# Performance work log

Measured on AMD Instinct MI355X. Metric: run time of the kernel, lower is better.

The kernel has to match this reference:

```python
import jax, jax.numpy as jnp
import numpy as np

EMBED_DIM = 1024
NUM_HEADS = 16
HEAD_DIM = EMBED_DIM // NUM_HEADS
B, T = 4, 1024
NEG = -1.0e9
LN_EPS = 1e-5


def setup_inputs() -> dict:
    key = jax.random.key(0)
    ks = jax.random.split(key, 13)
    s = 1.0 / np.sqrt(EMBED_DIM)
    return {
        "query": jax.random.normal(ks[0], (B, T, EMBED_DIM), jnp.float32),
        "key": jax.random.normal(ks[1], (B, T, EMBED_DIM), jnp.float32),
        "value": jax.random.normal(ks[2], (B, T, EMBED_DIM), jnp.float32),
        "mask": jax.random.randint(ks[3], (B, 1, T, T), 0, 2, jnp.int32),
        "Wq": jax.random.normal(ks[4], (EMBED_DIM, EMBED_DIM), jnp.float32) * s,
        "bq": jnp.zeros((EMBED_DIM,), jnp.float32),
        "Wk": jax.random.normal(ks[5], (EMBED_DIM, EMBED_DIM), jnp.float32) * s,
        "bk": jnp.zeros((EMBED_DIM,), jnp.float32),
        "Wv": jax.random.normal(ks[6], (EMBED_DIM, EMBED_DIM), jnp.float32) * s,
        "bv": jnp.zeros((EMBED_DIM,), jnp.float32),
        "Wo": jax.random.normal(ks[7], (EMBED_DIM, EMBED_DIM), jnp.float32) * s,
        "bo": jnp.zeros((EMBED_DIM,), jnp.float32),
        "gamma": jnp.ones((EMBED_DIM,), jnp.float32),
        "beta": jnp.zeros((EMBED_DIM,), jnp.float32),
    }


def _split_heads(x):
    # (B, T, E) -> (B, H, T, D)
    b, t, _ = x.shape
    return x.reshape(b, t, NUM_HEADS, HEAD_DIM).transpose(0, 2, 1, 3)


def _mha(query, key, value, mask, Wq, bq, Wk, bk, Wv, bv, Wo, bo, gamma, beta,
         temperature=1.0):
    q = _split_heads(query @ Wq.T + bq)
    k = _split_heads(key @ Wk.T + bk)
    v = _split_heads(value @ Wv.T + bv)
    # scores: (B, H, T, T)
    scale = jnp.sqrt(jnp.float32(HEAD_DIM)) * temperature
    scores = jnp.einsum("bhqd,bhkd->bhqk", q, k) / scale
    scores = jnp.where(mask == 0, NEG, scores)
    scores = scores - jnp.max(scores, axis=-1, keepdims=True)
    # temperature >= 0.01 in this config, so the low-temperature hard-cutoff
    # branch is skipped (matches torch's Python-level `if temperature < 0.01`).
    scores = jnp.nan_to_num(scores, nan=0.0, posinf=1.0e9, neginf=-1.0e9)
    attn = jax.nn.softmax(scores, axis=-1)
    # eval mode: dropout is identity (self.training is False)
    out = jnp.einsum("bhqk,bhkd->bhqd", attn, v)  # (B, H, T, D)
    out = out.transpose(0, 2, 1, 3).reshape(query.shape[0], query.shape[1], EMBED_DIM)
    out = out @ Wo.T + bo
    # layer norm over embed_dim
    mu = jnp.mean(out, axis=-1, keepdims=True)
    var = jnp.mean(jnp.square(out - mu), axis=-1, keepdims=True)
    out = (out - mu) * jax.lax.rsqrt(var + LN_EPS) * gamma + beta
    return out


def reference(query, key, value, mask, Wq, bq, Wk, bk, Wv, bv, Wo, bo, gamma, beta):
    return _mha(query, key, value, mask, Wq, bq, Wk, bk, Wv, bv, Wo, bo, gamma, beta)
```

## Files before the change

### kernel.cpp

```cpp
#include <hip/hip_runtime.h>
#include <cmath>

#define T_SEQ 1024
#define EMB   1024
#define NH    16
#define HD    64
#define NB    4
#define BQ    128
#define BK    64

#define QSCALE 0.18033688011112042f
#define BIAS2  -1.44269504e9f

using frag8   = __attribute__((ext_vector_type(8))) short;
using f32x4   = __attribute__((ext_vector_type(4))) float;
using short4v = __attribute__((ext_vector_type(4))) short;
using short8v = __attribute__((ext_vector_type(8))) short;

__device__ inline short f2bf(float f) {
    union { float f; unsigned u; } x; x.f = f;
    unsigned r = (x.u + 0x7FFFu + ((x.u >> 16) & 1u)) >> 16;
    return (short)r;
}
__device__ inline float bf2f(unsigned short u) {
    union { unsigned u; float f; } x; x.u = ((unsigned)u) << 16;
    return x.f;
}
__device__ inline int cvt_pk_bf16(float lo, float hi) {
    int r;
    asm("v_cvt_pk_bf16_f32 %0, %1, %2" : "=v"(r) : "v"(lo), "v"(hi));
    return r;
}

__device__ inline void glds16(const short* g, short* l) {
    __builtin_amdgcn_global_load_lds(
        (const __attribute__((address_space(1))) void*)g,
        (__attribute__((address_space(3))) void*)l, 16, 0, 0);
}

struct ConvArgs { const float* src[7]; short* dst[7]; int n8[7]; };

__global__ __launch_bounds__(256) void convert_bf16(ConvArgs a) {
    const int y = blockIdx.y;
    const int t = blockIdx.x * 256 + threadIdx.x;
    if (t >= a.n8[y]) return;
    const float4* s = (const float4*)a.src[y];
    const float4 v0 = s[t * 2], v1 = s[t * 2 + 1];
    short8v o;
    o[0] = f2bf(v0.x); o[1] = f2bf(v0.y); o[2] = f2bf(v0.z); o[3] = f2bf(v0.w);
    o[4] = f2bf(v1.x); o[5] = f2bf(v1.y); o[6] = f2bf(v1.z); o[7] = f2bf(v1.w);
    *(short8v*)&a.dst[y][t * 8] = o;
}

__global__ __launch_bounds__(256) void convert_mask(
    const int* __restrict__ mask, short* __restrict__ dst)
{
    const int wave = threadIdx.x >> 6, lane = threadIdx.x & 63;
    const int tile = blockIdx.x * 4 + wave;
    const int bb   = tile >> 12;
    const int q16  = (tile >> 6) & 63;
    const int k16  = tile & 63;
    const int qrow = lane >> 2;
    const int col4 = (lane & 3) * 4;
    const int4 mv = *(const int4*)&mask[((size_t)bb * T_SEQ + q16 * 16 + qrow) * T_SEQ
                                        + k16 * 16 + col4];
    const short BB = f2bf(BIAS2);
    short4v o;
    o[0] = mv.x ? (short)0 : BB;
    o[1] = mv.y ? (short)0 : BB;
    o[2] = mv.z ? (short)0 : BB;
    o[3] = mv.w ? (short)0 : BB;
    *(short4v*)&dst[(size_t)tile * 256 + qrow * 16 + col4] = o;
}

struct GemmB { const short* A; const short* W; const float* bias; short* out; float scale; };
struct QkvArgs { GemmB g[3]; };

template <int MODE>
__device__ inline void gemm_core(short* __restrict__ As,
                                 short* __restrict__ Bs,
                                 const short* __restrict__ A,
                                 const short* __restrict__ W,
                                 const float* __restrict__ bias,
                                 float scale,
                                 short* __restrict__ outS,
                                 float* __restrict__ outF,
                                 int m0, int n0, int k0, int kspan)
{
    const int tid  = threadIdx.x;
    const int wave = tid >> 6;
    const int lane = tid & 63;
    const int quad = lane >> 4;
    const int lm   = lane & 15;
    const int wr   = wave >> 1;
    const int wc   = wave & 1;
    const int K    = EMB;

    const int G0 = wave * 64 + lane, G1 = G0 + 256;
    const short* aSrc0 = A + (size_t)(m0 + (G0 >> 2)) * K + (G0 & 3) * 8;
    const short* aSrc1 = A + (size_t)(m0 + (G1 >> 2)) * K + (G1 & 3) * 8;
    const short* bSrc0 = W + (size_t)(n0 + (G0 >> 2)) * K + (G0 & 3) * 8;
    const short* bSrc1 = W + (size_t)(n0 + (G1 >> 2)) * K + (G1 & 3) * 8;
    short* aDst0 = As + wave * 512;
    short* aDst1 = As + 2048 + wave * 512;
    short* bDst0 = Bs + wave * 512;
    short* bDst1 = Bs + 2048 + wave * 512;

    f32x4 acc[4][4];
#pragma unroll
    for (int i = 0; i < 4; ++i)
#pragma unroll
        for (int j = 0; j < 4; ++j) acc[i][j] = (f32x4){0.f, 0.f, 0.f, 0.f};

    for (int kk = k0; kk < k0 + kspan; kk += 64) {
        __syncthreads();
        glds16(aSrc0 + kk,      aDst0);
        glds16(aSrc1 + kk,      aDst1);
        glds16(bSrc0 + kk,      bDst0);
        glds16(bSrc1 + kk,      bDst1);
        glds16(aSrc0 + kk + 32, aDst0 + 4096);
        glds16(aSrc1 + kk + 32, aDst1 + 4096);
        glds16(bSrc0 + kk + 32, bDst0 + 4096);
        glds16(bSrc1 + kk + 32, bDst1 + 4096);
        __syncthreads();

#pragma unroll
        for (int p = 0; p < 2; ++p) {
            frag8 aF[4], bF[4];
#pragma unroll
            for (int i = 0; i < 4; ++i)
                aF[i] = *(const frag8*)&As[p * 4096 + (wr * 64 + i * 16 + lm) * 32 + quad * 8];
#pragma unroll
            for (int j = 0; j < 4; ++j)
                bF[j] = *(const frag8*)&Bs[p * 4096 + (wc * 64 + j * 16 + lm) * 32 + quad * 8];
#pragma unroll
            for (int i = 0; i < 4; ++i)
#pragma unroll
                for (int j = 0; j < 4; ++j)
                    acc[i][j] = __builtin_amdgcn_mfma_f32_16x16x32_bf16(
                        aF[i], bF[j], acc[i][j], 0, 0, 0);
        }
    }

#pragma unroll
    for (int i = 0; i < 4; ++i)
#pragma unroll
        for (int j = 0; j < 4; ++j) {
            const int n = n0 + wc * 64 + j * 16 + lm;
            const float bv = (k0 == 0) ? bias[n] : 0.0f;
#pragma unroll
            for (int rr = 0; rr < 4; ++rr) {
                const int m = m0 + wr * 64 + i * 16 + quad * 4 + rr;
                const float val = (acc[i][j][rr] + bv) * scale;
                if (MODE == 0) {
                    outF[((size_t)(m >> 4) * 64 + (n >> 4)) * 256 +
                         rr * 64 + quad * 16 + lm] = val;
                } else {
                    const int bb = m >> 10, tt = m & 1023;
                    const int h = n >> 6,  d  = n & 63;
                    const size_t bh = (size_t)bb * NH + h;
                    if (MODE == 1) {
                        outS[((bh * 64 + (tt >> 4)) * 8 + (d >> 3)) * 128 +
                             (tt & 15) * 8 + (d & 7)] = f2bf(val);
                    } else {
                        outS[((((bh * 16 + (tt >> 6)) * 2 + ((tt >> 5) & 1)) * 4 +
                              (d >> 4)) * 4 + ((tt >> 2) & 3)) * 128 +
                             (d & 15) * 8 + (((tt & 16) >> 2) | (tt & 3))] = f2bf(val);
                    }
                }
            }
        }
}

__global__ __launch_bounds__(256, 4) void gemm_qkv(QkvArgs args) {
    __shared__ short As[2 * 128 * 32];
    __shared__ short Bs[2 * 128 * 32];
    const int id = blockIdx.x + 8 * blockIdx.y + 256 * blockIdx.z;
    const int a  = id & 7;
    const int k2 = id >> 3;
    const int nb = k2 & 7;
    const int c  = k2 >> 3;
    const int pair = a * 12 + c;
    const int mb = pair & 31;
    const int zb = pair >> 5;
    const GemmB g = args.g[zb];
    if (zb < 2) gemm_core<1>(As, Bs, g.A, g.W, g.bias, g.scale, g.out, nullptr,
                             mb * 128, nb * 128, 0, EMB);
    else        gemm_core<2>(As, Bs, g.A, g.W, g.bias, g.scale, g.out, nullptr,
                             mb * 128, nb * 128, 0, EMB);
}

__global__ __launch_bounds__(256, 4) void gemm_wo(const short* __restrict__ A,
                                                  const short* __restrict__ W,
                                                  const float* __restrict__ bias,
                                                  float* __restrict__ out0,
                                                  float* __restrict__ out1) {
    __shared__ short As[2 * 128 * 32];
    __shared__ short Bs[2 * 128 * 32];
    const int id = blockIdx.x + 8 * blockIdx.y;
    const int a  = id & 7;
    const int r  = id >> 3;
    const int nb = r & 7;
    const int pr = a * 8 + (r >> 3);
    const int mb = pr & 31;
    const int ks = pr >> 5;
    gemm_core<0>(As, Bs, A, W, bias, 1.0f, nullptr, ks ? out1 : out0,
                 mb * 128, nb * 128, ks * 512, 512);
}

__global__ __launch_bounds__(512, 4) void flash_attn_mfma(
    const short* __restrict__ qf_, const short* __restrict__ kf_,
    const short* __restrict__ vf_, const short* __restrict__ mf_,
    short* __restrict__ out)
{
    __shared__ short KV[2][2][4096];

    const int tid  = threadIdx.x;
    const int wave = tid >> 6;
    const int lane = tid & 63;
    const int quad = lane >> 4;
    const int lm   = lane & 15;

    const int id  = blockIdx.x;
    const int xcd = id & 7;
    const int idx = id >> 3;
    const int bh_i = xcd * 8 + (idx >> 3);
    const int b  = bh_i >> 4, h = bh_i & 15;
    const int qb = idx & 7;
    const int q0 = qb * BQ;
    const size_t bh = (size_t)bh_i;

    const short* sbase = ((wave < 4) ? kf_ : vf_) + bh * 65536
                         + (wave & 3) * 1024 + lane * 8;
    short* dstb = &KV[0][0][0] + (wave >> 2) * 4096 + (wave & 3) * 1024;

    const short* qb_ = qf_ + (bh * 64 + qb * 8 + wave) * 1024;
    const frag8 qfa = *(const frag8*)&qb_[(quad * 16 + lm) * 8];
    const frag8 qfb = *(const frag8*)&qb_[((quad + 4) * 16 + lm) * 8];

    const short* mrow = mf_ + ((size_t)b * 64 + qb * 8 + wave) * (64 * 256)
                        + lm * 16 + quad * 4;

    union { int i[4]; frag8 f; } ones;
    ones.i[0] = ones.i[1] = ones.i[2] = ones.i[3] = 0x3F803F80;

    f32x4 of[4];
#pragma unroll
    for (int dc = 0; dc < 4; ++dc) of[dc] = (f32x4){0.f, 0.f, 0.f, 0.f};
    f32x4 ls = (f32x4){0.f, 0.f, 0.f, 0.f};

    glds16(sbase,       dstb);
    glds16(sbase + 512, dstb + 512);
    short4v mb[4];
#pragma unroll
    for (int kc = 0; kc < 4; ++kc)
        mb[kc] = *(const short4v*)&mrow[kc * 256];
    __syncthreads();

    for (int kt = 0; kt < 16; ++kt) {
        const int cur = kt & 1;

        if (kt < 15) {
            short* nd = dstb + (cur ^ 1) * 8192;
            glds16(sbase + (kt + 1) * 4096,       nd);
            glds16(sbase + (kt + 1) * 4096 + 512, nd + 512);
        }
        short4v mc[4];
#pragma unroll
        for (int kc = 0; kc < 4; ++kc) mc[kc] = mb[kc];
        if (kt < 15) {
#pragma unroll
            for (int kc = 0; kc < 4; ++kc)
                mb[kc] = *(const short4v*)&mrow[((kt + 1) * 4 + kc) * 256];
        }

        f32x4 s[4];
#pragma unroll
        for (int kc = 0; kc < 4; ++kc) {
            const short* kb = &KV[cur][0][kc * 1024];
            const frag8 kfa = *(const frag8*)&kb[(quad * 16 + lm) * 8];
            const frag8 kfb = *(const frag8*)&kb[((quad + 4) * 16 + lm) * 8];
            f32x4 a = (f32x4){ bf2f((unsigned short)mc[kc][0]),
                               bf2f((unsigned short)mc[kc][1]),
                               bf2f((unsigned short)mc[kc][2]),
                               bf2f((unsigned short)mc[kc][3]) };
            a = __builtin_amdgcn_mfma_f32_16x16x32_bf16(kfa, qfa, a, 0, 0, 0);
            a = __builtin_amdgcn_mfma_f32_16x16x32_bf16(kfb, qfb, a, 0, 0, 0);
            s[kc] = a;
        }

#pragma unroll
        for (int kc = 0; kc < 4; ++kc) {
            s[kc][0] = exp2f(s[kc][0]); s[kc][1] = exp2f(s[kc][1]);
            s[kc][2] = exp2f(s[kc][2]); s[kc][3] = exp2f(s[kc][3]);
        }

        union { int i[4]; frag8 f; } ua, ub;
        ua.i[0] = cvt_pk_bf16(s[0][0], s[0][1]);
        ua.i[1] = cvt_pk_bf16(s[0][2], s[0][3]);
        ua.i[2] = cvt_pk_bf16(s[1][0], s[1][1]);
        ua.i[3] = cvt_pk_bf16(s[1][2], s[1][3]);
        ub.i[0] = cvt_pk_bf16(s[2][0], s[2][1]);
        ub.i[1] = cvt_pk_bf16(s[2][2], s[2][3]);
        ub.i[2] = cvt_pk_bf16(s[3][0], s[3][1]);
        ub.i[3] = cvt_pk_bf16(s[3][2], s[3][3]);

        __builtin_amdgcn_s_setprio(1);
#pragma unroll
        for (int dc = 0; dc < 4; ++dc) {
            const frag8 v0 = *(const frag8*)&KV[cur][1][(dc * 4 + quad) * 128 + lm * 8];
            const frag8 v1 = *(const frag8*)&KV[cur][1][((4 + dc) * 4 + quad) * 128 + lm * 8];
            of[dc] = __builtin_amdgcn_mfma_f32_16x16x32_bf16(v0, ua.f, of[dc], 0, 0, 0);
            of[dc] = __builtin_amdgcn_mfma_f32_16x16x32_bf16(v1, ub.f, of[dc], 0, 0, 0);
        }
        ls = __builtin_amdgcn_mfma_f32_16x16x32_bf16(ones.f, ua.f, ls, 0, 0, 0);
        ls = __builtin_amdgcn_mfma_f32_16x16x32_bf16(ones.f, ub.f, ls, 0, 0, 0);
        __builtin_amdgcn_s_setprio(0);

        __syncthreads();
    }

    const float inv = 1.0f / ls[0];

    short* ob = out + ((size_t)b * T_SEQ + q0 + wave * 16 + lm) * EMB + h * HD;
#pragma unroll
    for (int dc = 0; dc < 4; ++dc) {
        short4v o4;
#pragma unroll
        for (int rr = 0; rr < 4; ++rr) o4[rr] = f2bf(of[dc][rr] * inv);
        *(short4v*)&ob[dc * 16 + quad * 4] = o4;
    }
}

__global__ __launch_bounds__(256) void layernorm_k(
    const float* __restrict__ x0, const float* __restrict__ x1,
    const float* __restrict__ gamma, const float* __restrict__ beta,
    float* __restrict__ out)
{
    __shared__ float ws1[4], ws2[4];
    const int tid = threadIdx.x;
    const int row = blockIdx.x;
    const int m16 = row >> 4, rr = row & 3, qd = (row >> 2) & 3;

    const size_t ix = ((size_t)m16 * 64 + (tid >> 2)) * 256 +
                      rr * 64 + qd * 16 + (tid & 3) * 4;
    const float4 v1 = *(const float4*)&x0[ix];
    const float4 v2 = *(const float4*)&x1[ix];
    float4 v;
    v.x = v1.x + v2.x; v.y = v1.y + v2.y;
    v.z = v1.z + v2.z; v.w = v1.w + v2.w;

    float s  = v.x + v.y + v.z + v.w;
    float ss = v.x * v.x + v.y * v.y + v.z * v.z + v.w * v.w;
#pragma unroll
    for (int off = 32; off > 0; off >>= 1) {
        s  += __shfl_down(s, off);
        ss += __shfl_down(ss, off);
    }
    if ((tid & 63) == 0) { ws1[tid >> 6] = s; ws2[tid >> 6] = ss; }
    __syncthreads();
    if (tid == 0) {
        const float a = ws1[0] + ws1[1] + ws1[2] + ws1[3];
        const float bsum = ws2[0] + ws2[1] + ws2[2] + ws2[3];
        const float mu = a * (1.0f / EMB);
        const float var = bsum * (1.0f / EMB) - mu * mu;
        ws1[0] = mu;
        ws2[0] = rsqrtf(var + 1e-5f);
    }
    __syncthreads();
    const float mu = ws1[0], rstd = ws2[0];

    const float4 g = *(const float4*)&gamma[tid * 4];
    const float4 bt = *(const float4*)&beta[tid * 4];
    float4 r;
    r.x = (v.x - mu) * rstd * g.x + bt.x;
    r.y = (v.y - mu) * rstd * g.y + bt.y;
    r.z = (v.z - mu) * rstd * g.z + bt.z;
    r.w = (v.w - mu) * rstd * g.w + bt.w;
    *(float4*)&out[(size_t)row * EMB + tid * 4] = r;
}

extern "C" void kernel_launch(void* const* d_in, const int* in_sizes, int n_in,
                              void* d_out, int out_size, void* d_ws, size_t ws_size,
                              hipStream_t stream) {
    const float* query = (const float*)d_in[0];
    const float* key_i = (const float*)d_in[1];
    const float* value = (const float*)d_in[2];
    const int*   mask  = (const int*)d_in[3];
    const float* Wq = (const float*)d_in[4];
    const float* bq = (const float*)d_in[5];
    const float* Wk = (const float*)d_in[6];
    const float* bk = (const float*)d_in[7];
    const float* Wv = (const float*)d_in[8];
    const float* bv = (const float*)d_in[9];
    const float* Wo = (const float*)d_in[10];
    const float* bo = (const float*)d_in[11];
    const float* gamma = (const float*)d_in[12];
    const float* beta  = (const float*)d_in[13];

    const size_t SZ = (size_t)NB * T_SEQ * EMB;
    const size_t WZ = (size_t)EMB * EMB;
    short* sws = (short*)d_ws;
    short* q_bf  = sws;
    short* k_bf  = sws + SZ;
    short* v_bf  = sws + 2 * SZ;
    short* w_bf  = sws + 3 * SZ;
    short* qh    = sws + 4 * SZ;
    short* kh    = sws + 5 * SZ;
    short* vh    = sws + 6 * SZ;
    short* maskb = sws + 7 * SZ;
    short* attnb = q_bf;
    float* projb  = (float*)(sws + SZ);
    float* projb2 = (float*)(sws + 4 * SZ);

    ConvArgs ca;
    ca.src[0] = query; ca.dst[0] = q_bf;          ca.n8[0] = (int)(SZ / 8);
    ca.src[1] = key_i; ca.dst[1] = k_bf;          ca.n8[1] = (int)(SZ / 8);
    ca.src[2] = value; ca.dst[2] = v_bf;          ca.n8[2] = (int)(SZ / 8);
    ca.src[3] = Wq;    ca.dst[3] = w_bf;          ca.n8[3] = (int)(WZ / 8);
    ca.src[4] = Wk;    ca.dst[4] = w_bf + WZ;     ca.n8[4] = (int)(WZ / 8);
    ca.src[5] = Wv;    ca.dst[5] = w_bf + 2 * WZ; ca.n8[5] = (int)(WZ / 8);
    ca.src[6] = Wo;    ca.dst[6] = w_bf + 3 * WZ; ca.n8[6] = (int)(WZ / 8);
    convert_bf16<<<dim3((SZ / 8 + 255) / 256, 7), 256, 0, stream>>>(ca);

    convert_mask<<<dim3(NB * 64 * 64 / 4), 256, 0, stream>>>(mask, maskb);

    QkvArgs qa;
    qa.g[0] = { q_bf, w_bf,          bq, qh, QSCALE };
    qa.g[1] = { k_bf, w_bf + WZ,     bk, kh, 1.0f };
    qa.g[2] = { v_bf, w_bf + 2 * WZ, bv, vh, 1.0f };
    gemm_qkv<<<dim3(EMB / 128, NB * T_SEQ / 128, 3), 256, 0, stream>>>(qa);

    flash_attn_mfma<<<dim3(T_SEQ / BQ * NH * NB), 512, 0, stream>>>(qh, kh, vh, maskb, attnb);

    gemm_wo<<<dim3(8, 64), 256, 0, stream>>>(attnb, w_bf + 3 * WZ, bo, projb, projb2);

    layernorm_k<<<dim3(NB * T_SEQ), 256, 0, stream>>>(projb, projb2, gamma, beta, (float*)d_out);
}
```

Baseline: 233.1 us.

## Double-buffer GEMM LDS loads and compact bf16 conversion grid

The GEMM main loop now prefetches the next 32-wide K slice into the alternate LDS buffer while MFMAs run on the current one. This replaces the old pattern of two barriers around a bulk load, so global-to-LDS latency can overlap with compute. The conversion kernel also switches from a 2D grid, where most blocks for the small weight matrices exited early, to a 1D grid sized exactly to the work. The risk is that one barrier per 32-K step may be too little to order the async global_load_lds writes correctly.

```diff
diff --git a/kernel.cpp b/kernel.cpp
--- a/kernel.cpp
+++ b/kernel.cpp
@@ -38,12 +38,13 @@
         (__attribute__((address_space(3))) void*)l, 16, 0, 0);
 }
 
-struct ConvArgs { const float* src[7]; short* dst[7]; int n8[7]; };
+struct ConvArgs { const float* src[7]; short* dst[7]; };
 
 __global__ __launch_bounds__(256) void convert_bf16(ConvArgs a) {
-    const int y = blockIdx.y;
-    const int t = blockIdx.x * 256 + threadIdx.x;
-    if (t >= a.n8[y]) return;
+    const int bid = blockIdx.x;
+    int y, t;
+    if (bid < 6144) { y = bid >> 11;            t = ((bid & 2047) << 8) | threadIdx.x; }
+    else { const int r = bid - 6144; y = 3 + (r >> 9); t = ((r & 511) << 8) | threadIdx.x; }
     const float4* s = (const float4*)a.src[y];
     const float4 v0 = s[t * 2], v1 = s[t * 2 + 1];
     short8v o;
@@ -101,10 +102,6 @@
     const short* aSrc1 = A + (size_t)(m0 + (G1 >> 2)) * K + (G1 & 3) * 8;
     const short* bSrc0 = W + (size_t)(n0 + (G0 >> 2)) * K + (G0 & 3) * 8;
     const short* bSrc1 = W + (size_t)(n0 + (G1 >> 2)) * K + (G1 & 3) * 8;
-    short* aDst0 = As + wave * 512;
-    short* aDst1 = As + 2048 + wave * 512;
-    short* bDst0 = Bs + wave * 512;
-    short* bDst1 = Bs + 2048 + wave * 512;
 
     f32x4 acc[4][4];
 #pragma unroll
@@ -112,34 +109,41 @@
 #pragma unroll
         for (int j = 0; j < 4; ++j) acc[i][j] = (f32x4){0.f, 0.f, 0.f, 0.f};
 
-    for (int kk = k0; kk < k0 + kspan; kk += 64) {
+    const int NP = kspan >> 5;
+
+    glds16(aSrc0 + k0, As + wave * 512);
+    glds16(aSrc1 + k0, As + 2048 + wave * 512);
+    glds16(bSrc0 + k0, Bs + wave * 512);
+    glds16(bSrc1 + k0, Bs + 2048 + wave * 512);
+    __syncthreads();
+
+    for (int t = 0; t < NP; ++t) {
+        const int cur = (t & 1) * 4096;
+
+        if (t + 1 < NP) {
+            const int off = k0 + (t + 1) * 32;
+            const int par = 4096 - cur;
+            glds16(aSrc0 + off, As + par + wave * 512);
+            glds16(aSrc1 + off, As + par + 2048 + wave * 512);
+            glds16(bSrc0 + off, Bs + par + wave * 512);
+            glds16(bSrc1 + off, Bs + par + 2048 + wave * 512);
+        }
+
+        frag8 aF[4], bF[4];
+#pragma unroll
+        for (int i = 0; i < 4; ++i)
+            aF[i] = *(const frag8*)&As[cur + (wr * 64 + i * 16 + lm) * 32 + quad * 8];
+#pragma unroll
+        for (int j = 0; j < 4; ++j)
+            bF[j] = *(const frag8*)&Bs[cur + (wc * 64 + j * 16 + lm) * 32 + quad * 8];
+#pragma unroll
+        for (int i = 0; i < 4; ++i)
+#pragma unroll
+            for (int j = 0; j < 4; ++j)
+                acc[i][j] = __builtin_amdgcn_mfma_f32_16x16x32_bf16(
+                    aF[i], bF[j], acc[i][j], 0, 0, 0);
+
         __syncthreads();
-        glds16(aSrc0 + kk,      aDst0);
-        glds16(aSrc1 + kk,      aDst1);
-        glds16(bSrc0 + kk,      bDst0);
-        glds16(bSrc1 + kk,      bDst1);
-        glds16(aSrc0 + kk + 32, aDst0 + 4096);
-        glds16(aSrc1 + kk + 32, aDst1 + 4096);
-        glds16(bSrc0 + kk + 32, bDst0 + 4096);
-        glds16(bSrc1 + kk + 32, bDst1 + 4096);
-        __syncthreads();
-
-#pragma unroll
-        for (int p = 0; p < 2; ++p) {
-            frag8 aF[4], bF[4];
-#pragma unroll
-            for (int i = 0; i < 4; ++i)
-                aF[i] = *(const frag8*)&As[p * 4096 + (wr * 64 + i * 16 + lm) * 32 + quad * 8];
-#pragma unroll
-            for (int j = 0; j < 4; ++j)
-                bF[j] = *(const frag8*)&Bs[p * 4096 + (wc * 64 + j * 16 + lm) * 32 + quad * 8];
-#pragma unroll
-            for (int i = 0; i < 4; ++i)
-#pragma unroll
-                for (int j = 0; j < 4; ++j)
-                    acc[i][j] = __builtin_amdgcn_mfma_f32_16x16x32_bf16(
-                        aF[i], bF[j], acc[i][j], 0, 0, 0);
-        }
     }
 
 #pragma unroll
@@ -414,14 +418,14 @@
     float* projb2 = (float*)(sws + 4 * SZ);
 
     ConvArgs ca;
-    ca.src[0] = query; ca.dst[0] = q_bf;          ca.n8[0] = (int)(SZ / 8);
-    ca.src[1] = key_i; ca.dst[1] = k_bf;          ca.n8[1] = (int)(SZ / 8);
-    ca.src[2] = value; ca.dst[2] = v_bf;          ca.n8[2] = (int)(SZ / 8);
-    ca.src[3] = Wq;    ca.dst[3] = w_bf;          ca.n8[3] = (int)(WZ / 8);
-    ca.src[4] = Wk;    ca.dst[4] = w_bf + WZ;     ca.n8[4] = (int)(WZ / 8);
-    ca.src[5] = Wv;    ca.dst[5] = w_bf + 2 * WZ; ca.n8[5] = (int)(WZ / 8);
-    ca.src[6] = Wo;    ca.dst[6] = w_bf + 3 * WZ; ca.n8[6] = (int)(WZ / 8);
-    convert_bf16<<<dim3((SZ / 8 + 255) / 256, 7), 256, 0, stream>>>(ca);
+    ca.src[0] = query; ca.dst[0] = q_bf;
+    ca.src[1] = key_i; ca.dst[1] = k_bf;
+    ca.src[2] = value; ca.dst[2] = v_bf;
+    ca.src[3] = Wq;    ca.dst[3] = w_bf;
+    ca.src[4] = Wk;    ca.dst[4] = w_bf + WZ;
+    ca.src[5] = Wv;    ca.dst[5] = w_bf + 2 * WZ;
+    ca.src[6] = Wo;    ca.dst[6] = w_bf + 3 * WZ;
+    convert_bf16<<<dim3(8192), 256, 0, stream>>>(ca);
 
     convert_mask<<<dim3(NB * 64 * 64 / 4), 256, 0, stream>>>(mask, maskb);
 
```

After: 238.1 us. 2.2% more time.
